# Performance work log

Measured on AMD Instinct MI355X. Metric: run time of the kernel, lower is better.

## Reference

```python
import jax, jax.numpy as jnp
import numpy as np

B, S, D, H = 2, 2048, 1024, 16
HD = D // H  # head_dim = 64


def setup_inputs() -> dict:
    key = jax.random.key(0)
    ks = jax.random.split(key, 11)
    init = 1.0 / np.sqrt(D)
    inp = {
        "query": jax.random.normal(ks[0], (B, S, D), jnp.float32),
        "key": jax.random.normal(ks[1], (B, S, D), jnp.float32),
        "value": jax.random.normal(ks[2], (B, S, D), jnp.float32),
        "Wq": jax.random.uniform(ks[3], (D, D), jnp.float32, -init, init),
        "bq": jax.random.uniform(ks[4], (D,), jnp.float32, -init, init),
        "Wk": jax.random.uniform(ks[5], (D, D), jnp.float32, -init, init),
        "bk": jax.random.uniform(ks[6], (D,), jnp.float32, -init, init),
        "Wv": jax.random.uniform(ks[7], (D, D), jnp.float32, -init, init),
        "bv": jax.random.uniform(ks[8], (D,), jnp.float32, -init, init),
        "Wo": jax.random.uniform(ks[9], (D, D), jnp.float32, -init, init),
        "bo": jax.random.uniform(ks[10], (D,), jnp.float32, -init, init),
    }
    return inp


def reference(query, key, value, Wq, bq, Wk, bk, Wv, bv, Wo, bo):
    # Linear projections (torch Linear: x @ W.T + b)
    q = query @ Wq.T + bq  # [B,S,D]
    k = key @ Wk.T + bk
    v = value @ Wv.T + bv
    # split heads -> [B,H,S,HD]
    q = q.reshape(B, S, H, HD).transpose(0, 2, 1, 3)
    k = k.reshape(B, S, H, HD).transpose(0, 2, 1, 3)
    v = v.reshape(B, S, H, HD).transpose(0, 2, 1, 3)
    # NOTE: original code divides by scale = head_dim**-0.5, i.e. multiplies
    # scores by sqrt(head_dim). Reproduced faithfully.
    scale = HD ** (-0.5)
    scores = jnp.einsum("bhqd,bhkd->bhqk", q, k) / scale  # [B,H,S,S]
    attn = jax.nn.softmax(scores, axis=-1)
    x = jnp.einsum("bhqk,bhkd->bhqd", attn, v)  # [B,H,S,HD]
    x = x.transpose(0, 2, 1, 3).reshape(B, S, D)
    return x @ Wo.T + bo
```

## Files before the change

### kernel.cpp

```cpp
#include <hip/hip_runtime.h>
#include <stdint.h>
#include <stddef.h>

#define SCALE_LOG2E 11.541560327111707f
#define E8 4194304
#define M1 1048576

typedef __attribute__((ext_vector_type(8))) _Float16 f16x8;
typedef __attribute__((ext_vector_type(4))) _Float16 f16x4;
typedef __attribute__((ext_vector_type(4))) float f32x4;

#if __has_builtin(__builtin_amdgcn_exp2f)
#define EXP2F(x) __builtin_amdgcn_exp2f(x)
#else
#define EXP2F(x) exp2f(x)
#endif

__device__ __forceinline__ f32x4 mfma_f16(f16x8 a, f16x8 b, f32x4 c) {
  return __builtin_amdgcn_mfma_f32_16x16x32_f16(a, b, c, 0, 0, 0);
}

__device__ __forceinline__ f32x4 mfma16_f16(f16x4 a, f16x4 b, f32x4 c) {
  return __builtin_amdgcn_mfma_f32_16x16x16f16(a, b, c, 0, 0, 0);
}

__device__ __forceinline__ void async16(const void* g, void* lds) {
  __builtin_amdgcn_global_load_lds(
      (const __attribute__((address_space(1))) unsigned int*)g,
      (__attribute__((address_space(3))) unsigned int*)lds, 16, 0, 0);
}

__global__ void prep_all(const float* __restrict__ q, const float* __restrict__ k,
                         const float* __restrict__ v,
                         const float* __restrict__ wq, const float* __restrict__ wk,
                         const float* __restrict__ wv, const float* __restrict__ wo,
                         _Float16* __restrict__ Xf, _Float16* __restrict__ Wf) {
  const int gid = blockIdx.x;
  const float* src;
  _Float16* dst;
  int i;
  if (gid < 6144) {
    const int z = gid >> 11;
    src = (z == 0) ? q : (z == 1) ? k : v;
    dst = Xf + (size_t)z * E8;
    i = (gid & 2047) * 512 + threadIdx.x;
  } else {
    const int g2 = gid - 6144;
    const int z = g2 >> 9;
    src = (z == 0) ? wq : (z == 1) ? wk : (z == 2) ? wv : wo;
    dst = Wf + (size_t)z * M1;
    i = (g2 & 511) * 512 + threadIdx.x;
  }
#pragma unroll
  for (int off = 0; off < 512; off += 256) {
    float4 x = ((const float4*)src)[i + off];
    f16x4 h = {(_Float16)x.x, (_Float16)x.y, (_Float16)x.z, (_Float16)x.w};
    ((f16x4*)dst)[i + off] = h;
  }
}

__global__ __launch_bounds__(256, 3) void gemm_qkv(
    const _Float16* __restrict__ Xf,
    const _Float16* __restrict__ Wf,
    const float* __restrict__ bq, const float* __restrict__ bk,
    const float* __restrict__ bv,
    _Float16* __restrict__ Of)
{
  __shared__ _Float16 SMEM[16384];
  _Float16* LA = SMEM;
  _Float16* LB = SMEM + 8192;
  const int z = blockIdx.z;
  const int tid = threadIdx.x;
  const int lane = tid & 63;
  const int wv = tid >> 6;
  const int wm = wv >> 1, wn = wv & 1;
  const int rl = lane & 15, qd = lane >> 4;
  const int m0 = blockIdx.x * 128, n0 = blockIdx.y * 128;

  const _Float16* A0 = Xf + (size_t)z * E8;
  const _Float16* W0 = Wf + (size_t)z * M1;
  const float* bias = (z == 0) ? bq : (z == 1) ? bk : bv;

  f32x4 acc[4][4];
#pragma unroll
  for (int i = 0; i < 4; i++)
#pragma unroll
    for (int j = 0; j < 4; j++) acc[i][j] = f32x4{0.f, 0.f, 0.f, 0.f};

  const int srow = wv * 32 + (lane >> 2);
  const int scol = (lane & 3) * 8;

  auto stage = [&](int k0, int buf) {
    const _Float16* ga = A0 + (size_t)(m0 + srow) * 1024 + k0 + scol;
    async16(ga, &LA[buf * 4096 + wv * 1024]);
    async16(ga + 16 * 1024, &LA[buf * 4096 + wv * 1024 + 512]);
    const _Float16* gb = W0 + (size_t)(n0 + srow) * 1024 + k0 + scol;
    async16(gb, &LB[buf * 4096 + wv * 1024]);
    async16(gb + 16 * 1024, &LB[buf * 4096 + wv * 1024 + 512]);
  };

  stage(0, 0);
  for (int t = 0; t < 32; t++) {
    const int buf = t & 1;
    __syncthreads();
    if (t + 1 < 32) stage((t + 1) * 32, buf ^ 1);
    f16x8 af[4], bfr[4];
#pragma unroll
    for (int i = 0; i < 4; i++) af[i] = *(const f16x8*)&LA[buf * 4096 + (wm * 64 + i * 16 + rl) * 32 + qd * 8];
#pragma unroll
    for (int j = 0; j < 4; j++) bfr[j] = *(const f16x8*)&LB[buf * 4096 + (wn * 64 + j * 16 + rl) * 32 + qd * 8];
#pragma unroll
    for (int i = 0; i < 4; i++)
#pragma unroll
      for (int j = 0; j < 4; j++) acc[i][j] = mfma_f16(af[i], bfr[j], acc[i][j]);
  }

  if (z == 2) {
    __syncthreads();
#pragma unroll
    for (int j = 0; j < 4; j++) {
      const int nl = wn * 64 + j * 16 + rl;
      const float bj = bias[n0 + nl];
      const int xsw = (nl & 7) << 4;
#pragma unroll
      for (int i = 0; i < 4; i++) {
        const int ml = wm * 64 + i * 16 + qd * 4;
        f16x4 pk = {(_Float16)(acc[i][j][0] + bj), (_Float16)(acc[i][j][1] + bj),
                    (_Float16)(acc[i][j][2] + bj), (_Float16)(acc[i][j][3] + bj)};
        *(f16x4*)&SMEM[nl * 128 + (ml ^ xsw)] = pk;
      }
    }
    __syncthreads();
    const int b = m0 >> 11, s0 = m0 & 2047;
    _Float16* base = Of + 2 * (size_t)E8;
#pragma unroll
    for (int it2 = 0; it2 < 8; it2++) {
      const int n = (it2 * 256 + tid) >> 4;
      const int m8 = (tid & 15) * 8;
      f16x8 vrow = *(const f16x8*)&SMEM[n * 128 + (m8 ^ ((n & 7) << 4))];
      const int nn = n0 + n;
      const int hh = nn >> 6, e = nn & 63;
      *(f16x8*)(base + (((size_t)((b * 16 + hh) * 64 + e)) << 11) + s0 + m8) = vrow;
    }
  } else {
    const float scl = (z == 0) ? SCALE_LOG2E : 1.0f;
    _Float16* base = Of + (size_t)z * E8;
    __syncthreads();
#pragma unroll
    for (int j = 0; j < 4; j++) {
      const int nl = wn * 64 + j * 16 + rl;
      const float bj = bias[n0 + nl];
#pragma unroll
      for (int i = 0; i < 4; i++) {
        const int ml = wm * 64 + i * 16 + qd * 4;
        const int np = nl ^ (qd << 4);
#pragma unroll
        for (int r = 0; r < 4; r++)
          SMEM[(ml + r) * 128 + np] = (_Float16)((acc[i][j][r] + bj) * scl);
      }
    }
    __syncthreads();
#pragma unroll
    for (int it2 = 0; it2 < 8; it2++) {
      const int m = (it2 * 256 + tid) >> 4;
      const int col8 = (tid & 15) * 8;
      const int np = col8 ^ (((m >> 2) & 3) << 4);
      f16x8 vrow = *(const f16x8*)&SMEM[m * 128 + np];
      const int sg = m0 + m;
      const int b = sg >> 11, s = sg & 2047;
      const int nn = n0 + col8;
      const int hh = nn >> 6, e = nn & 63;
      *(f16x8*)(base + (((size_t)((b * 16 + hh) * 2048 + s)) << 6) + e) = vrow;
    }
  }
}

__global__ __launch_bounds__(512, 4) void attn_kernel(
    const _Float16* __restrict__ Qb,
    const _Float16* __restrict__ Kb,
    const _Float16* __restrict__ Vt,
    _Float16* __restrict__ Xo)
{
  __shared__ _Float16 Ks[2][4096];
  __shared__ _Float16 Vs[2][4096];
  const int tid = threadIdx.x;
  const int lane = tid & 63;
  const int wv = tid >> 6;
  const int rl = lane & 15, qd = lane >> 4;
  const int bh = blockIdx.x;
  const int q0 = blockIdx.y * 128 + wv * 16;

  f16x8 qf[2];
#pragma unroll
  for (int kk = 0; kk < 2; kk++)
    qf[kk] = *(const f16x8*)(Qb + ((size_t)bh * 2048 + q0 + rl) * 64 + kk * 32 + qd * 8);

  float m_ = -1e30f, l_ = 0.f;
  f32x4 o[4];
#pragma unroll
  for (int jt = 0; jt < 4; jt++) o[jt] = f32x4{0.f, 0.f, 0.f, 0.f};

  auto stage = [&](int kv, int buf) {
    const int row = tid >> 3;
    const int c = (tid & 7) ^ (row & 7);
    async16(Kb + ((size_t)bh * 2048 + kv + row) * 64 + c * 8, &Ks[buf][wv * 512]);
    async16(Vt + ((size_t)bh * 64 + row) * 2048 + kv + c * 8, &Vs[buf][wv * 512]);
  };

  stage(0, 0);

  for (int t = 0; t < 32; t++) {
    const int buf = t & 1;
    __syncthreads();
    if (t + 1 < 32) stage((t + 1) * 64, buf ^ 1);

    f32x4 sc[4];
#pragma unroll
    for (int nt = 0; nt < 4; nt++) sc[nt] = f32x4{0.f, 0.f, 0.f, 0.f};
    __builtin_amdgcn_s_setprio(1);
#pragma unroll
    for (int nt = 0; nt < 4; nt++) {
      const int ro = (nt * 16 + rl) * 64;
#pragma unroll
      for (int kk = 0; kk < 2; kk++) {
        const int cc = (((kk * 4 + qd) ^ (rl & 7)) << 3);
        f16x8 kh = *(const f16x8*)&Ks[buf][ro + cc];
        sc[nt] = mfma_f16(kh, qf[kk], sc[nt]);
      }
    }
    __builtin_amdgcn_s_setprio(0);

    f16x4 pf[4];
    {
      float a0 = fmaxf(fmaxf(sc[0][0], sc[0][1]), fmaxf(sc[0][2], sc[0][3]));
      float a1 = fmaxf(fmaxf(sc[1][0], sc[1][1]), fmaxf(sc[1][2], sc[1][3]));
      float a2 = fmaxf(fmaxf(sc[2][0], sc[2][1]), fmaxf(sc[2][2], sc[2][3]));
      float a3 = fmaxf(fmaxf(sc[3][0], sc[3][1]), fmaxf(sc[3][2], sc[3][3]));
      float mloc = fmaxf(fmaxf(a0, a1), fmaxf(a2, a3));
      float mx = fmaxf(mloc, __shfl_xor(mloc, 16));
      mx = fmaxf(mx, __shfl_xor(mx, 32));
      const float mold = m_;
      float mnew = mold;
      if (__any(mx > mold + 8.f)) {
        mnew = fmaxf(mold, mx);
        const float al = EXP2F(mold - mnew);
        l_ *= al;
#pragma unroll
        for (int jt = 0; jt < 4; jt++)
#pragma unroll
          for (int r = 0; r < 4; r++) o[jt][r] *= al;
        m_ = mnew;
      }
      float sm = 0.f;
#pragma unroll
      for (int nt = 0; nt < 4; nt++) {
        const float p0 = EXP2F(sc[nt][0] - mnew);
        const float p1 = EXP2F(sc[nt][1] - mnew);
        const float p2 = EXP2F(sc[nt][2] - mnew);
        const float p3 = EXP2F(sc[nt][3] - mnew);
        sm += (p0 + p1) + (p2 + p3);
        pf[nt] = f16x4{(_Float16)p0, (_Float16)p1, (_Float16)p2, (_Float16)p3};
      }
      l_ += sm;
    }

    __builtin_amdgcn_s_setprio(1);
#pragma unroll
    for (int nt = 0; nt < 4; nt++) {
      const int cb = nt * 2 + (qd >> 1);
#pragma unroll
      for (int jt = 0; jt < 4; jt++) {
        const int row = jt * 16 + rl;
        f16x4 vvv = *(const f16x4*)&Vs[buf][row * 64 + ((cb ^ (rl & 7)) << 3) + (qd & 1) * 4];
        o[jt] = mfma16_f16(vvv, pf[nt], o[jt]);
      }
    }
    __builtin_amdgcn_s_setprio(0);
  }

  {
    float lt = l_ + __shfl_xor(l_, 16);
    lt += __shfl_xor(lt, 32);
    const float inv = 1.0f / lt;
    const int b = bh >> 4, hh = bh & 15;
    const int s = q0 + rl;
    _Float16* xp = Xo + ((size_t)(b * 2048 + s)) * 1024 + hh * 64;
#pragma unroll
    for (int jt = 0; jt < 4; jt++) {
      f16x4 pk = {(_Float16)(o[jt][0] * inv), (_Float16)(o[jt][1] * inv),
                  (_Float16)(o[jt][2] * inv), (_Float16)(o[jt][3] * inv)};
      *(f16x4*)(xp + jt * 16 + qd * 4) = pk;
    }
  }
}

__global__ __launch_bounds__(256, 2) void gemm_out(
    const _Float16* __restrict__ A0,
    const _Float16* __restrict__ W0,
    const float* __restrict__ bias,
    float* __restrict__ out)
{
  __shared__ _Float16 LA[2][2048];
  __shared__ _Float16 LB[2][4096];
  const int tid = threadIdx.x;
  const int lane = tid & 63;
  const int wv = tid >> 6;
  const int wm = wv >> 1, wn = wv & 1;
  const int rl = lane & 15, qd = lane >> 4;
  const int m0 = blockIdx.x * 64, n0 = blockIdx.y * 128;

  f32x4 acc[2][4];
#pragma unroll
  for (int i = 0; i < 2; i++)
#pragma unroll
    for (int j = 0; j < 4; j++) acc[i][j] = f32x4{0.f, 0.f, 0.f, 0.f};

  auto stage = [&](int k0, int buf) {
    {
      const int row = tid >> 2, c = tid & 3;
      async16(A0 + (size_t)(m0 + row) * 1024 + k0 + c * 8, &LA[buf][wv * 512]);
    }
#pragma unroll
    for (int it = 0; it < 2; it++) {
      const int cI = it * 256 + tid;
      const int row = cI >> 2, c = cI & 3;
      async16(W0 + (size_t)(n0 + row) * 1024 + k0 + c * 8,
              &LB[buf][it * 2048 + wv * 512]);
    }
  };

  stage(0, 0);
  for (int t = 0; t < 32; t++) {
    const int buf = t & 1;
    __syncthreads();
    if (t + 1 < 32) stage((t + 1) * 32, buf ^ 1);
    f16x8 af[2], bfr[4];
#pragma unroll
    for (int i = 0; i < 2; i++) af[i] = *(const f16x8*)&LA[buf][(wm * 32 + i * 16 + rl) * 32 + qd * 8];
#pragma unroll
    for (int j = 0; j < 4; j++) bfr[j] = *(const f16x8*)&LB[buf][(wn * 64 + j * 16 + rl) * 32 + qd * 8];
#pragma unroll
    for (int i = 0; i < 2; i++)
#pragma unroll
      for (int j = 0; j < 4; j++) acc[i][j] = mfma_f16(af[i], bfr[j], acc[i][j]);
  }

#pragma unroll
  for (int j = 0; j < 4; j++) {
    const int nn = n0 + wn * 64 + j * 16 + rl;
    const float bj = bias[nn];
#pragma unroll
    for (int i = 0; i < 2; i++) {
      const int mm = m0 + wm * 32 + i * 16 + qd * 4;
#pragma unroll
      for (int r = 0; r < 4; r++)
        out[(size_t)(mm + r) * 1024 + nn] = acc[i][j][r] + bj;
    }
  }
}

extern "C" void kernel_launch(void* const* d_in, const int* in_sizes, int n_in,
                              void* d_out, int out_size, void* d_ws, size_t ws_size,
                              hipStream_t stream) {
  const float* query = (const float*)d_in[0];
  const float* key   = (const float*)d_in[1];
  const float* value = (const float*)d_in[2];
  const float* Wq = (const float*)d_in[3];
  const float* bq = (const float*)d_in[4];
  const float* Wk = (const float*)d_in[5];
  const float* bk = (const float*)d_in[6];
  const float* Wv = (const float*)d_in[7];
  const float* bv = (const float*)d_in[8];
  const float* Wo = (const float*)d_in[9];
  const float* bo = (const float*)d_in[10];

  _Float16* ws = (_Float16*)d_ws;
  _Float16* Xf = ws;
  _Float16* Wf = ws + 3 * (size_t)E8;
  _Float16* Qh = Wf + 4 * (size_t)M1;
  _Float16* Kh = Qh + (size_t)E8;
  _Float16* Vt = Kh + (size_t)E8;
  _Float16* Xa = Vt + (size_t)E8;

  prep_all<<<8192, 256, 0, stream>>>(query, key, value, Wq, Wk, Wv, Wo, Xf, Wf);
  gemm_qkv<<<dim3(32, 8, 3), 256, 0, stream>>>(Xf, Wf, bq, bk, bv, Qh);
  attn_kernel<<<dim3(32, 16), 512, 0, stream>>>(Qh, Kh, Vt, Xa);
  gemm_out<<<dim3(64, 8), 256, 0, stream>>>(Xa, Wf + 3 * (size_t)M1, bo, (float*)d_out);
}
```

Before: 230.9 us.

## Fuse fp32-to-fp16 activation conversion into QKV GEMM staging

Drops the separate conversion pass over the query/key/value activations. The QKV GEMM now stages fp32 tiles directly into LDS with a swizzled async load and converts them to fp16 while building the MFMA operands; only the weights are still pre-converted. This removes a full write and re-read of three fp16 activation tensors, but doubles the LDS footprint for the A tile and adds conversion work inside the GEMM main loop, which may reduce occupancy.

```diff
diff --git a/kernel.cpp b/kernel.cpp
--- a/kernel.cpp
+++ b/kernel.cpp
@@ -30,29 +30,16 @@
       (__attribute__((address_space(3))) unsigned int*)lds, 16, 0, 0);
 }
 
-__global__ void prep_all(const float* __restrict__ q, const float* __restrict__ k,
-                         const float* __restrict__ v,
-                         const float* __restrict__ wq, const float* __restrict__ wk,
-                         const float* __restrict__ wv, const float* __restrict__ wo,
-                         _Float16* __restrict__ Xf, _Float16* __restrict__ Wf) {
+__global__ void prep_w(const float* __restrict__ wq, const float* __restrict__ wk,
+                       const float* __restrict__ wv, const float* __restrict__ wo,
+                       _Float16* __restrict__ Wf) {
   const int gid = blockIdx.x;
-  const float* src;
-  _Float16* dst;
-  int i;
-  if (gid < 6144) {
-    const int z = gid >> 11;
-    src = (z == 0) ? q : (z == 1) ? k : v;
-    dst = Xf + (size_t)z * E8;
-    i = (gid & 2047) * 512 + threadIdx.x;
-  } else {
-    const int g2 = gid - 6144;
-    const int z = g2 >> 9;
-    src = (z == 0) ? wq : (z == 1) ? wk : (z == 2) ? wv : wo;
-    dst = Wf + (size_t)z * M1;
-    i = (g2 & 511) * 512 + threadIdx.x;
-  }
-#pragma unroll
-  for (int off = 0; off < 512; off += 256) {
+  const int z = gid >> 8;
+  const float* src = (z == 0) ? wq : (z == 1) ? wk : (z == 2) ? wv : wo;
+  _Float16* dst = Wf + (size_t)z * M1;
+  const int i = (gid & 255) * 1024 + threadIdx.x;
+#pragma unroll
+  for (int off = 0; off < 1024; off += 256) {
     float4 x = ((const float4*)src)[i + off];
     f16x4 h = {(_Float16)x.x, (_Float16)x.y, (_Float16)x.z, (_Float16)x.w};
     ((f16x4*)dst)[i + off] = h;
@@ -60,15 +47,15 @@
 }
 
 __global__ __launch_bounds__(256, 3) void gemm_qkv(
-    const _Float16* __restrict__ Xf,
+    const float* __restrict__ q32, const float* __restrict__ k32,
+    const float* __restrict__ v32,
     const _Float16* __restrict__ Wf,
     const float* __restrict__ bq, const float* __restrict__ bk,
     const float* __restrict__ bv,
     _Float16* __restrict__ Of)
 {
-  __shared__ _Float16 SMEM[16384];
-  _Float16* LA = SMEM;
-  _Float16* LB = SMEM + 8192;
+  __shared__ float LAf[8192];
+  __shared__ _Float16 LB[8192];
   const int z = blockIdx.z;
   const int tid = threadIdx.x;
   const int lane = tid & 63;
@@ -77,7 +64,7 @@
   const int rl = lane & 15, qd = lane >> 4;
   const int m0 = blockIdx.x * 128, n0 = blockIdx.y * 128;
 
-  const _Float16* A0 = Xf + (size_t)z * E8;
+  const float* A32 = (z == 0) ? q32 : (z == 1) ? k32 : v32;
   const _Float16* W0 = Wf + (size_t)z * M1;
   const float* bias = (z == 0) ? bq : (z == 1) ? bk : bv;
 
@@ -90,23 +77,41 @@
   const int srow = wv * 32 + (lane >> 2);
   const int scol = (lane & 3) * 8;
 
-  auto stage = [&](int k0, int buf) {
-    const _Float16* ga = A0 + (size_t)(m0 + srow) * 1024 + k0 + scol;
-    async16(ga, &LA[buf * 4096 + wv * 1024]);
-    async16(ga + 16 * 1024, &LA[buf * 4096 + wv * 1024 + 512]);
+  auto stageA = [&](int k0, int buf) {
+#pragma unroll
+    for (int j = 0; j < 4; j++) {
+      const int cI = j * 256 + tid;
+      const int row = cI >> 3, s = cI & 7;
+      const int c = (s & 1) | ((((s >> 1) & 3) ^ (row & 3)) << 1);
+      async16(A32 + (size_t)(m0 + row) * 1024 + k0 + c * 4,
+              &LAf[buf * 4096 + (j * 256 + wv * 64) * 4]);
+    }
+  };
+  auto stageB = [&](int k0, int buf) {
     const _Float16* gb = W0 + (size_t)(n0 + srow) * 1024 + k0 + scol;
     async16(gb, &LB[buf * 4096 + wv * 1024]);
     async16(gb + 16 * 1024, &LB[buf * 4096 + wv * 1024 + 512]);
   };
 
-  stage(0, 0);
+  stageA(0, 0);
+  stageB(0, 0);
   for (int t = 0; t < 32; t++) {
     const int buf = t & 1;
     __syncthreads();
-    if (t + 1 < 32) stage((t + 1) * 32, buf ^ 1);
+    if (t + 1 < 32) {
+      stageA((t + 1) * 32, buf ^ 1);
+      stageB((t + 1) * 32, buf ^ 1);
+    }
     f16x8 af[4], bfr[4];
 #pragma unroll
-    for (int i = 0; i < 4; i++) af[i] = *(const f16x8*)&LA[buf * 4096 + (wm * 64 + i * 16 + rl) * 32 + qd * 8];
+    for (int i = 0; i < 4; i++) {
+      const int R = wm * 64 + i * 16 + rl;
+      const int sp = (qd ^ (R & 3)) << 3;
+      f32x4 lo = *(const f32x4*)&LAf[buf * 4096 + R * 32 + sp];
+      f32x4 hi = *(const f32x4*)&LAf[buf * 4096 + R * 32 + sp + 4];
+      af[i] = f16x8{(_Float16)lo[0], (_Float16)lo[1], (_Float16)lo[2], (_Float16)lo[3],
+                    (_Float16)hi[0], (_Float16)hi[1], (_Float16)hi[2], (_Float16)hi[3]};
+    }
 #pragma unroll
     for (int j = 0; j < 4; j++) bfr[j] = *(const f16x8*)&LB[buf * 4096 + (wn * 64 + j * 16 + rl) * 32 + qd * 8];
 #pragma unroll
@@ -114,6 +119,8 @@
 #pragma unroll
       for (int j = 0; j < 4; j++) acc[i][j] = mfma_f16(af[i], bfr[j], acc[i][j]);
   }
+
+  _Float16* Ct = (_Float16*)LAf;
 
   if (z == 2) {
     __syncthreads();
@@ -127,7 +134,7 @@
         const int ml = wm * 64 + i * 16 + qd * 4;
         f16x4 pk = {(_Float16)(acc[i][j][0] + bj), (_Float16)(acc[i][j][1] + bj),
                     (_Float16)(acc[i][j][2] + bj), (_Float16)(acc[i][j][3] + bj)};
-        *(f16x4*)&SMEM[nl * 128 + (ml ^ xsw)] = pk;
+        *(f16x4*)&Ct[nl * 128 + (ml ^ xsw)] = pk;
       }
     }
     __syncthreads();
@@ -137,7 +144,7 @@
     for (int it2 = 0; it2 < 8; it2++) {
       const int n = (it2 * 256 + tid) >> 4;
       const int m8 = (tid & 15) * 8;
-      f16x8 vrow = *(const f16x8*)&SMEM[n * 128 + (m8 ^ ((n & 7) << 4))];
+      f16x8 vrow = *(const f16x8*)&Ct[n * 128 + (m8 ^ ((n & 7) << 4))];
       const int nn = n0 + n;
       const int hh = nn >> 6, e = nn & 63;
       *(f16x8*)(base + (((size_t)((b * 16 + hh) * 64 + e)) << 11) + s0 + m8) = vrow;
@@ -156,7 +163,7 @@
         const int np = nl ^ (qd << 4);
 #pragma unroll
         for (int r = 0; r < 4; r++)
-          SMEM[(ml + r) * 128 + np] = (_Float16)((acc[i][j][r] + bj) * scl);
+          Ct[(ml + r) * 128 + np] = (_Float16)((acc[i][j][r] + bj) * scl);
       }
     }
     __syncthreads();
@@ -165,7 +172,7 @@
       const int m = (it2 * 256 + tid) >> 4;
       const int col8 = (tid & 15) * 8;
       const int np = col8 ^ (((m >> 2) & 3) << 4);
-      f16x8 vrow = *(const f16x8*)&SMEM[m * 128 + np];
+      f16x8 vrow = *(const f16x8*)&Ct[m * 128 + np];
       const int sg = m0 + m;
       const int b = sg >> 11, s = sg & 2047;
       const int nn = n0 + col8;
@@ -375,15 +382,14 @@
   const float* bo = (const float*)d_in[10];
 
   _Float16* ws = (_Float16*)d_ws;
-  _Float16* Xf = ws;
   _Float16* Wf = ws + 3 * (size_t)E8;
   _Float16* Qh = Wf + 4 * (size_t)M1;
   _Float16* Kh = Qh + (size_t)E8;
   _Float16* Vt = Kh + (size_t)E8;
   _Float16* Xa = Vt + (size_t)E8;
 
-  prep_all<<<8192, 256, 0, stream>>>(query, key, value, Wq, Wk, Wv, Wo, Xf, Wf);
-  gemm_qkv<<<dim3(32, 8, 3), 256, 0, stream>>>(Xf, Wf, bq, bk, bv, Qh);
+  prep_w<<<1024, 256, 0, stream>>>(Wq, Wk, Wv, Wo, Wf);
+  gemm_qkv<<<dim3(32, 8, 3), 256, 0, stream>>>(query, key, value, Wf, bq, bk, bv, Qh);
   attn_kernel<<<dim3(32, 16), 512, 0, stream>>>(Qh, Kh, Vt, Xa);
   gemm_out<<<dim3(64, 8), 256, 0, stream>>>(Xa, Wf + 3 * (size_t)M1, bo, (float*)d_out);
 }
```

New measurement: 251.5 us. 1.09x slower.
